# Kernel tuning notes

Measured on AMD Instinct MI355X. Metric: run time of the kernel, lower is better.

## Reference

```python
import jax, jax.numpy as jnp
import numpy as np

IMG_DIM = 512


def _grid_q(img_dim):
    # matches torch module: q = [repeat(x, D), tile(y, D)] -> shape [2, D*D]
    x = np.arange(img_dim)
    q = np.stack([np.repeat(x, img_dim), np.tile(x, img_dim)], axis=0)
    return jnp.asarray(q, jnp.float32)


def _get_pixel(point, neighbor, imflat, img_dim):
    # point, neighbor: [N,2,HW]; imflat: [N,3,HW]
    w = 1.0 - jnp.abs(point - neighbor)          # [N,2,HW]
    weight = w[:, 0] * w[:, 1]                   # [N,HW]
    inds = (neighbor[:, 1] + img_dim * neighbor[:, 0]).astype(jnp.int32)  # y + D*x, [N,HW]
    # fused gather over all 3 channels (original does 3 separate torch.gather)
    pix = jnp.take_along_axis(imflat, inds[:, None, :], axis=2)  # [N,3,HW]
    return weight[:, None, :] * pix


def _get_masked_rp(image, mask, qi_orig, img_dim):
    N, Cc, H, W = image.shape
    imflat = image.reshape(N, Cc, H * W)
    qi_rescale = qi_orig * img_dim
    qi = jnp.clip(qi_rescale, 0.001, img_dim - 1.001)
    xf = jnp.floor(qi[:, 0:1]); yf = jnp.floor(qi[:, 1:2])
    xc = jnp.ceil(qi[:, 0:1]);  yc = jnp.ceil(qi[:, 1:2])
    res = (_get_pixel(qi, jnp.concatenate([xf, yf], axis=1), imflat, img_dim)
         + _get_pixel(qi, jnp.concatenate([xc, yf], axis=1), imflat, img_dim)
         + _get_pixel(qi, jnp.concatenate([xf, yc], axis=1), imflat, img_dim)
         + _get_pixel(qi, jnp.concatenate([xc, yc], axis=1), imflat, img_dim))
    oob_loss = jnp.mean((qi_rescale - qi) ** 2) / (img_dim ** 2) * 0.0001
    res_img = res.reshape(image.shape)
    return res_img * mask, oob_loss  # mask broadcasts [N,1,H,W] -> [N,3,H,W]


def setup_inputs() -> dict:
    key = jax.random.key(0)
    k1, k2, k3, k4, k5 = jax.random.split(key, 5)
    N, D = 16, IMG_DIM
    im1 = jax.random.normal(k1, (N, 3, D, D), dtype=jnp.float32)
    im2 = jax.random.normal(k2, (N, 3, D, D), dtype=jnp.float32)
    C = jax.random.normal(k3, (N, 2, D, D), dtype=jnp.float32)
    M1 = jax.random.uniform(k4, (N, 1, D, D), dtype=jnp.float32)
    M2 = jax.random.uniform(k5, (N, 1, D, D), dtype=jnp.float32)
    return {"im1": im1, "im2": im2, "C": C, "M1": M1, "M2": M2}


def reference(im1, im2, C, M1, M2):
    img_dim = im1.shape[-1]
    N = C.shape[0]
    Cflat = C.reshape(N, 2, -1)                 # [N,2,HW]
    total_mask = M1 + M2
    M1n = M1 / total_mask
    M2n = M2 / total_mask
    q = _grid_q(img_dim)[None]                  # [1,2,HW], broadcasts to [N,2,HW]
    a, oob_a = _get_masked_rp(im1, M1n, q + Cflat, img_dim)
    b, oob_b = _get_masked_rp(im2, M2n, q - Cflat, img_dim)
    return a + b, oob_a + oob_b
```

## Files before the change

### kernel.cpp

```cpp
#include <hip/hip_runtime.h>

#define D     512
#define HW    (D * D)
#define BLOCK 256
#define ROWS  4
#define COLS  256

__device__ __forceinline__ void sample1(const float* __restrict__ im,
                                        const float* __restrict__ cpix,
                                        float rx, float ry, float m,
                                        float r[3], float* oob) {
    float cxq = fminf(fmaxf(rx, 0.001f), 510.999f);
    float cyq = fminf(fmaxf(ry, 0.001f), 510.999f);
    float dx = rx - cxq;
    float dy = ry - cyq;
    *oob += dx * dx + dy * dy;

    float xf = floorf(cxq), xc = ceilf(cxq);
    float yf = floorf(cyq), yc = ceilf(cyq);
    float wxf = 1.0f - (cxq - xf);
    float wxc = 1.0f - (xc - cxq);
    float wyf = 1.0f - (cyq - yf);
    float wyc = 1.0f - (yc - cyq);
    float w00 = wxf * wyf, w10 = wxc * wyf, w01 = wxf * wyc, w11 = wxc * wyc;

    float p[3][4];
#pragma unroll
    for (int c = 0; c < 3; ++c) {
        p[c][0] = cpix[c * 4 + 0];
        p[c][1] = cpix[c * 4 + 1];
        p[c][2] = cpix[c * 4 + 2];
        p[c][3] = cpix[c * 4 + 3];
    }

    bool corner = (rx >= 510.999f) && (ry >= 510.999f);
    if (!corner) {
        int ixf = (int)xf, ixc = (int)xc, iyf = (int)yf, iyc = (int)yc;
        int i00 = iyf + D * ixf;
        int i10 = iyf + D * ixc;
        int i01 = iyc + D * ixf;
        int i11 = iyc + D * ixc;
#pragma unroll
        for (int c = 0; c < 3; ++c) {
            const float* __restrict__ ch = im + (size_t)c * HW;
            p[c][0] = ch[i00];
            p[c][1] = ch[i10];
            p[c][2] = ch[i01];
            p[c][3] = ch[i11];
        }
    }

#pragma unroll
    for (int c = 0; c < 3; ++c)
        r[c] += m * (w00 * p[c][0] + w10 * p[c][1] + w01 * p[c][2] + w11 * p[c][3]);
}

__global__ void __launch_bounds__(BLOCK) vm_kernel(
    const float* __restrict__ im1, const float* __restrict__ im2,
    const float* __restrict__ C,   const float* __restrict__ M1,
    const float* __restrict__ M2,  float* __restrict__ out,
    double* __restrict__ partials)
{
    int b    = blockIdx.x;
    int colh = b & 1;
    int rg   = (b >> 1) & 127;
    int n    = b >> 8;
    int j    = colh * COLS + threadIdx.x;
    int i0   = rg * ROWS;

    const float* base1 = im1 + (size_t)n * 3 * HW;
    const float* base2 = im2 + (size_t)n * 3 * HW;

    float cp1[12], cp2[12];
#pragma unroll
    for (int c = 0; c < 3; ++c) {
        const float* c1 = base1 + (size_t)c * HW;
        const float* c2 = base2 + (size_t)c * HW;
        cp1[c * 4 + 0] = c1[510 + D * 510];
        cp1[c * 4 + 1] = c1[510 + D * 511];
        cp1[c * 4 + 2] = c1[511 + D * 510];
        cp1[c * 4 + 3] = c1[511 + D * 511];
        cp2[c * 4 + 0] = c2[510 + D * 510];
        cp2[c * 4 + 1] = c2[510 + D * 511];
        cp2[c * 4 + 2] = c2[511 + D * 510];
        cp2[c * 4 + 3] = c2[511 + D * 511];
    }

    const size_t cb = (size_t)n * 2 * HW;
    const size_t mb = (size_t)n * HW;
    const size_t ob = (size_t)n * 3 * HW;

    float oob = 0.0f;

#pragma unroll
    for (int r = 0; r < ROWS; ++r) {
        int i = i0 + r;
        size_t pp = (size_t)i * D + j;

        float cx = C[cb + pp];
        float cy = C[cb + HW + pp];
        float m1 = M1[mb + pp];
        float m2 = M2[mb + pp];
        float tot = m1 + m2;
        float m1n = m1 / tot;
        float m2n = m2 / tot;

        float acc[3] = {0.f, 0.f, 0.f};
        float fi = (float)i, fj = (float)j;
        sample1(base1, cp1, (fi + cx) * (float)D, (fj + cy) * (float)D, m1n, acc, &oob);
        sample1(base2, cp2, (fi - cx) * (float)D, (fj - cy) * (float)D, m2n, acc, &oob);

        out[ob + pp]          = acc[0];
        out[ob + HW + pp]     = acc[1];
        out[ob + 2 * HW + pp] = acc[2];
    }

    for (int off = 32; off > 0; off >>= 1)
        oob += __shfl_down(oob, off, 64);

    __shared__ float soob[BLOCK / 64];
    int lane = threadIdx.x & 63;
    int w    = threadIdx.x >> 6;
    if (lane == 0) soob[w] = oob;
    __syncthreads();
    if (threadIdx.x == 0)
        partials[blockIdx.x] = (double)soob[0] + (double)soob[1]
                             + (double)soob[2] + (double)soob[3];
}

__global__ void __launch_bounds__(BLOCK) reduce_kernel(
    const double* __restrict__ partials, int nparts,
    float* __restrict__ out_last, double scale)
{
    double s = 0.0;
    for (int i = threadIdx.x; i < nparts; i += BLOCK)
        s += partials[i];
    for (int off = 32; off > 0; off >>= 1)
        s += __shfl_down(s, off, 64);

    __shared__ double sm[BLOCK / 64];
    int lane = threadIdx.x & 63;
    int w    = threadIdx.x >> 6;
    if (lane == 0) sm[w] = s;
    __syncthreads();
    if (threadIdx.x == 0)
        *out_last = (float)((sm[0] + sm[1] + sm[2] + sm[3]) * scale);
}

extern "C" void kernel_launch(void* const* d_in, const int* in_sizes, int n_in,
                              void* d_out, int out_size, void* d_ws, size_t ws_size,
                              hipStream_t stream) {
    const float* im1 = (const float*)d_in[0];
    const float* im2 = (const float*)d_in[1];
    const float* C   = (const float*)d_in[2];
    const float* M1  = (const float*)d_in[3];
    const float* M2  = (const float*)d_in[4];
    float* out = (float*)d_out;
    double* ws = (double*)d_ws;

    int N = in_sizes[3] / HW;
    int blocks = N * (D / ROWS) * (D / COLS);

    vm_kernel<<<blocks, BLOCK, 0, stream>>>(im1, im2, C, M1, M2, out, ws);

    double scale = 1.0 / ((double)N * 2.0 * (double)HW) / (double)HW * 1e-4;
    reduce_kernel<<<1, BLOCK, 0, stream>>>(ws, blocks, out + (out_size - 1), scale);
}
```

Measured before the change: 210.8 us.

## Vectorize per-thread loads and take a wave-uniform corner fast path

Each thread now handles 8 consecutive columns of one row. It reads C, M1 and M2 and writes the output as float4 vectors. A wave-wide ballot decides whether every lane's samples clamp to the bottom-right corner; if so, the wave uses the preloaded corner pixels and skips all gather address math and per-lane branching. The first 8 columns of each row go to extra tail blocks that run the scalar gather path. The aim is fewer memory transactions and less divergence, at the cost of more registers and a more complex block layout.

```diff
diff --git a/kernel.cpp b/kernel.cpp
--- a/kernel.cpp
+++ b/kernel.cpp
@@ -3,116 +3,175 @@
 #define D     512
 #define HW    (D * D)
 #define BLOCK 256
-#define ROWS  4
-#define COLS  256
-
-__device__ __forceinline__ void sample1(const float* __restrict__ im,
-                                        const float* __restrict__ cpix,
-                                        float rx, float ry, float m,
-                                        float r[3], float* oob) {
-    float cxq = fminf(fmaxf(rx, 0.001f), 510.999f);
-    float cyq = fminf(fmaxf(ry, 0.001f), 510.999f);
-    float dx = rx - cxq;
-    float dy = ry - cyq;
+
+__device__ __forceinline__ void weights_oob(float rx, float ry,
+    float& w00, float& w10, float& w01, float& w11,
+    float& cxq, float& cyq, float* oob)
+{
+    cxq = fminf(fmaxf(rx, 0.001f), 510.999f);
+    cyq = fminf(fmaxf(ry, 0.001f), 510.999f);
+    float dx = rx - cxq, dy = ry - cyq;
     *oob += dx * dx + dy * dy;
-
     float xf = floorf(cxq), xc = ceilf(cxq);
     float yf = floorf(cyq), yc = ceilf(cyq);
-    float wxf = 1.0f - (cxq - xf);
-    float wxc = 1.0f - (xc - cxq);
-    float wyf = 1.0f - (cyq - yf);
-    float wyc = 1.0f - (yc - cyq);
-    float w00 = wxf * wyf, w10 = wxc * wyf, w01 = wxf * wyc, w11 = wxc * wyc;
-
-    float p[3][4];
+    float wxf = 1.0f - (cxq - xf), wxc = 1.0f - (xc - cxq);
+    float wyf = 1.0f - (cyq - yf), wyc = 1.0f - (yc - cyq);
+    w00 = wxf * wyf; w10 = wxc * wyf; w01 = wxf * wyc; w11 = wxc * wyc;
+}
+
+__device__ __forceinline__ void samp_gather(const float* __restrict__ im,
+    float rx, float ry, float m, float r3[3], float* oob)
+{
+    float w00, w10, w01, w11, cxq, cyq;
+    weights_oob(rx, ry, w00, w10, w01, w11, cxq, cyq, oob);
+    int xf = (int)cxq, yf = (int)cyq;
+    int xc = (int)ceilf(cxq), yc = (int)ceilf(cyq);
+    int i00 = yf + D * xf, i10 = yf + D * xc;
+    int i01 = yc + D * xf, i11 = yc + D * xc;
 #pragma unroll
     for (int c = 0; c < 3; ++c) {
-        p[c][0] = cpix[c * 4 + 0];
-        p[c][1] = cpix[c * 4 + 1];
-        p[c][2] = cpix[c * 4 + 2];
-        p[c][3] = cpix[c * 4 + 3];
+        const float* __restrict__ ch = im + (size_t)c * HW;
+        r3[c] += m * (w00 * ch[i00] + w10 * ch[i10] + w01 * ch[i01] + w11 * ch[i11]);
     }
-
-    bool corner = (rx >= 510.999f) && (ry >= 510.999f);
-    if (!corner) {
-        int ixf = (int)xf, ixc = (int)xc, iyf = (int)yf, iyc = (int)yc;
-        int i00 = iyf + D * ixf;
-        int i10 = iyf + D * ixc;
-        int i01 = iyc + D * ixf;
-        int i11 = iyc + D * ixc;
-#pragma unroll
-        for (int c = 0; c < 3; ++c) {
-            const float* __restrict__ ch = im + (size_t)c * HW;
-            p[c][0] = ch[i00];
-            p[c][1] = ch[i10];
-            p[c][2] = ch[i01];
-            p[c][3] = ch[i11];
-        }
-    }
-
+}
+
+__device__ __forceinline__ void samp_corner(const float* __restrict__ cp,
+    float rx, float ry, float m, float r3[3], float* oob)
+{
+    float w00, w10, w01, w11, cxq, cyq;
+    weights_oob(rx, ry, w00, w10, w01, w11, cxq, cyq, oob);
 #pragma unroll
     for (int c = 0; c < 3; ++c)
-        r[c] += m * (w00 * p[c][0] + w10 * p[c][1] + w01 * p[c][2] + w11 * p[c][3]);
+        r3[c] += m * (w00 * cp[c * 4 + 0] + w10 * cp[c * 4 + 1]
+                    + w01 * cp[c * 4 + 2] + w11 * cp[c * 4 + 3]);
 }
 
 __global__ void __launch_bounds__(BLOCK) vm_kernel(
     const float* __restrict__ im1, const float* __restrict__ im2,
     const float* __restrict__ C,   const float* __restrict__ M1,
     const float* __restrict__ M2,  float* __restrict__ out,
-    double* __restrict__ partials)
-{
-    int b    = blockIdx.x;
-    int colh = b & 1;
-    int rg   = (b >> 1) & 127;
-    int n    = b >> 8;
-    int j    = colh * COLS + threadIdx.x;
-    int i0   = rg * ROWS;
-
-    const float* base1 = im1 + (size_t)n * 3 * HW;
-    const float* base2 = im2 + (size_t)n * 3 * HW;
-
-    float cp1[12], cp2[12];
-#pragma unroll
-    for (int c = 0; c < 3; ++c) {
-        const float* c1 = base1 + (size_t)c * HW;
-        const float* c2 = base2 + (size_t)c * HW;
-        cp1[c * 4 + 0] = c1[510 + D * 510];
-        cp1[c * 4 + 1] = c1[510 + D * 511];
-        cp1[c * 4 + 2] = c1[511 + D * 510];
-        cp1[c * 4 + 3] = c1[511 + D * 511];
-        cp2[c * 4 + 0] = c2[510 + D * 510];
-        cp2[c * 4 + 1] = c2[510 + D * 511];
-        cp2[c * 4 + 2] = c2[511 + D * 510];
-        cp2[c * 4 + 3] = c2[511 + D * 511];
-    }
-
-    const size_t cb = (size_t)n * 2 * HW;
-    const size_t mb = (size_t)n * HW;
-    const size_t ob = (size_t)n * 3 * HW;
-
+    double* __restrict__ partials, int nblk_a)
+{
     float oob = 0.0f;
-
-#pragma unroll
-    for (int r = 0; r < ROWS; ++r) {
-        int i = i0 + r;
+    int b = blockIdx.x;
+
+    if (b < nblk_a) {
+        int n  = b >> 7;
+        int rg = b & 127;
+        int r  = threadIdx.x >> 6;
+        int l  = threadIdx.x & 63;
+        int i  = rg * 4 + r;
+        bool active = (l < 63);
+        int j0 = 8 + l * 8;
+
+        const float* base1 = im1 + (size_t)n * 3 * HW;
+        const float* base2 = im2 + (size_t)n * 3 * HW;
+
+        float cp1[12], cp2[12];
+#pragma unroll
+        for (int c = 0; c < 3; ++c) {
+            const float* c1 = base1 + (size_t)c * HW;
+            const float* c2 = base2 + (size_t)c * HW;
+            cp1[c*4+0] = c1[510 + D*510]; cp1[c*4+1] = c1[510 + D*511];
+            cp1[c*4+2] = c1[511 + D*510]; cp1[c*4+3] = c1[511 + D*511];
+            cp2[c*4+0] = c2[510 + D*510]; cp2[c*4+1] = c2[510 + D*511];
+            cp2[c*4+2] = c2[511 + D*510]; cp2[c*4+3] = c2[511 + D*511];
+        }
+
+        size_t cb = (size_t)n * 2 * HW, mb = (size_t)n * HW, ob = (size_t)n * 3 * HW;
+        size_t row = (size_t)i * D + j0;
+
+        float cx[8], cy[8], m1n[8], m2n[8];
+        bool lane_bad = false;
+        if (active) {
+            float4 cxa = *(const float4*)(C  + cb + row);
+            float4 cxb = *(const float4*)(C  + cb + row + 4);
+            float4 cya = *(const float4*)(C  + cb + HW + row);
+            float4 cyb = *(const float4*)(C  + cb + HW + row + 4);
+            float4 m1a = *(const float4*)(M1 + mb + row);
+            float4 m1b = *(const float4*)(M1 + mb + row + 4);
+            float4 m2a = *(const float4*)(M2 + mb + row);
+            float4 m2b = *(const float4*)(M2 + mb + row + 4);
+            cx[0]=cxa.x; cx[1]=cxa.y; cx[2]=cxa.z; cx[3]=cxa.w;
+            cx[4]=cxb.x; cx[5]=cxb.y; cx[6]=cxb.z; cx[7]=cxb.w;
+            cy[0]=cya.x; cy[1]=cya.y; cy[2]=cya.z; cy[3]=cya.w;
+            cy[4]=cyb.x; cy[5]=cyb.y; cy[6]=cyb.z; cy[7]=cyb.w;
+            float m1v[8] = {m1a.x,m1a.y,m1a.z,m1a.w,m1b.x,m1b.y,m1b.z,m1b.w};
+            float m2v[8] = {m2a.x,m2a.y,m2a.z,m2a.w,m2b.x,m2b.y,m2b.z,m2b.w};
+            float fi = (float)i;
+#pragma unroll
+            for (int k = 0; k < 8; ++k) {
+                float tot = m1v[k] + m2v[k];
+                m1n[k] = m1v[k] / tot;
+                m2n[k] = m2v[k] / tot;
+                float mx = (fi - fabsf(cx[k])) * 512.0f;
+                float my = ((float)(j0 + k) - fabsf(cy[k])) * 512.0f;
+                lane_bad |= (mx < 510.5f) || (my < 510.5f);
+            }
+        } else {
+#pragma unroll
+            for (int k = 0; k < 8; ++k) { cx[k]=0.f; cy[k]=0.f; m1n[k]=0.f; m2n[k]=0.f; }
+        }
+
+        unsigned long long bad = __ballot(lane_bad);
+        float a0[8], a1[8], a2[8];
+#pragma unroll
+        for (int k = 0; k < 8; ++k) { a0[k]=0.f; a1[k]=0.f; a2[k]=0.f; }
+        float fi = (float)i;
+
+        if (bad == 0ULL) {
+            if (active) {
+#pragma unroll
+                for (int k = 0; k < 8; ++k) {
+                    float fj = (float)(j0 + k);
+                    float r3[3] = {0.f, 0.f, 0.f};
+                    samp_corner(cp1, (fi + cx[k]) * 512.0f, (fj + cy[k]) * 512.0f, m1n[k], r3, &oob);
+                    samp_corner(cp2, (fi - cx[k]) * 512.0f, (fj - cy[k]) * 512.0f, m2n[k], r3, &oob);
+                    a0[k] = r3[0]; a1[k] = r3[1]; a2[k] = r3[2];
+                }
+            }
+        } else {
+            if (active) {
+#pragma unroll
+                for (int k = 0; k < 8; ++k) {
+                    float fj = (float)(j0 + k);
+                    float r3[3] = {0.f, 0.f, 0.f};
+                    samp_gather(base1, (fi + cx[k]) * 512.0f, (fj + cy[k]) * 512.0f, m1n[k], r3, &oob);
+                    samp_gather(base2, (fi - cx[k]) * 512.0f, (fj - cy[k]) * 512.0f, m2n[k], r3, &oob);
+                    a0[k] = r3[0]; a1[k] = r3[1]; a2[k] = r3[2];
+                }
+            }
+        }
+
+        if (active) {
+            *(float4*)(out + ob + row)            = make_float4(a0[0],a0[1],a0[2],a0[3]);
+            *(float4*)(out + ob + row + 4)        = make_float4(a0[4],a0[5],a0[6],a0[7]);
+            *(float4*)(out + ob + HW + row)       = make_float4(a1[0],a1[1],a1[2],a1[3]);
+            *(float4*)(out + ob + HW + row + 4)   = make_float4(a1[4],a1[5],a1[6],a1[7]);
+            *(float4*)(out + ob + 2*HW + row)     = make_float4(a2[0],a2[1],a2[2],a2[3]);
+            *(float4*)(out + ob + 2*HW + row + 4) = make_float4(a2[4],a2[5],a2[6],a2[7]);
+        }
+    } else {
+        int t = (b - nblk_a) * BLOCK + threadIdx.x;
+        int n   = t >> 12;
+        int rem = t & 4095;
+        int i = rem >> 3, j = rem & 7;
+        const float* base1 = im1 + (size_t)n * 3 * HW;
+        const float* base2 = im2 + (size_t)n * 3 * HW;
+        size_t cb = (size_t)n * 2 * HW, mb = (size_t)n * HW, ob = (size_t)n * 3 * HW;
         size_t pp = (size_t)i * D + j;
 
-        float cx = C[cb + pp];
-        float cy = C[cb + HW + pp];
-        float m1 = M1[mb + pp];
-        float m2 = M2[mb + pp];
-        float tot = m1 + m2;
-        float m1n = m1 / tot;
-        float m2n = m2 / tot;
-
-        float acc[3] = {0.f, 0.f, 0.f};
+        float cxv = C[cb + pp], cyv = C[cb + HW + pp];
+        float m1v = M1[mb + pp], m2v = M2[mb + pp];
+        float tot = m1v + m2v;
+        float m1nv = m1v / tot, m2nv = m2v / tot;
+        float r3[3] = {0.f, 0.f, 0.f};
         float fi = (float)i, fj = (float)j;
-        sample1(base1, cp1, (fi + cx) * (float)D, (fj + cy) * (float)D, m1n, acc, &oob);
-        sample1(base2, cp2, (fi - cx) * (float)D, (fj - cy) * (float)D, m2n, acc, &oob);
-
-        out[ob + pp]          = acc[0];
-        out[ob + HW + pp]     = acc[1];
-        out[ob + 2 * HW + pp] = acc[2];
+        samp_gather(base1, (fi + cxv) * 512.0f, (fj + cyv) * 512.0f, m1nv, r3, &oob);
+        samp_gather(base2, (fi - cxv) * 512.0f, (fj - cyv) * 512.0f, m2nv, r3, &oob);
+        out[ob + pp]          = r3[0];
+        out[ob + HW + pp]     = r3[1];
+        out[ob + 2 * HW + pp] = r3[2];
     }
 
     for (int off = 32; off > 0; off >>= 1)
@@ -159,9 +218,11 @@
     double* ws = (double*)d_ws;
 
     int N = in_sizes[3] / HW;
-    int blocks = N * (D / ROWS) * (D / COLS);
-
-    vm_kernel<<<blocks, BLOCK, 0, stream>>>(im1, im2, C, M1, M2, out, ws);
+    int nblk_a = N * 128;
+    int nblk_b = N * 16;
+    int blocks = nblk_a + nblk_b;
+
+    vm_kernel<<<blocks, BLOCK, 0, stream>>>(im1, im2, C, M1, M2, out, ws, nblk_a);
 
     double scale = 1.0 / ((double)N * 2.0 * (double)HW) / (double)HW * 1e-4;
     reduce_kernel<<<1, BLOCK, 0, stream>>>(ws, blocks, out + (out_size - 1), scale);
```

After: 227.3 us. +7.8%, slower.
